# Kernel tuning notes

Hardware: AMD Instinct MI355X
Metric: run time of the kernel (lower is better)

## Reference

```python
import jax, jax.numpy as jnp
import numpy as np

K, T, F = 30000, 48, 4
EPS = 1e-5  # torch BatchNorm1d default eps


def _bn_params(key, c):
    k1, k2, k3, k4 = jax.random.split(key, 4)
    g = jax.random.uniform(k1, (c,), jnp.float32, 0.5, 1.5)
    b = jax.random.normal(k2, (c,), jnp.float32) * 0.1
    m = jax.random.normal(k3, (c,), jnp.float32) * 0.1
    v = jax.random.uniform(k4, (c,), jnp.float32, 0.5, 1.5)
    return g, b, m, v


def setup_inputs() -> dict:
    key = jax.random.key(0)
    ks = jax.random.split(key, 12)
    features = jax.random.normal(ks[0], (K, T, F), jnp.float32)
    # at least 1 valid point per non-empty voxel
    num_voxels = jnp.maximum(jax.random.randint(ks[1], (K,), 0, T), 1).astype(jnp.int32)
    coors = jax.random.randint(ks[2], (K, 3), 0, 100).astype(jnp.int32)
    # VFE1: in=8 (4 + 3 rel + 1 dist), units = 32//2 = 16
    w1 = jax.random.normal(ks[3], (8, 16), jnp.float32) / np.sqrt(8)
    b1 = jax.random.normal(ks[4], (16,), jnp.float32) * 0.01
    g1, be1, m1, v1 = _bn_params(ks[5], 16)
    # VFE2: in=32, units = 128//2 = 64
    w2 = jax.random.normal(ks[6], (32, 64), jnp.float32) / np.sqrt(32)
    b2 = jax.random.normal(ks[7], (64,), jnp.float32) * 0.01
    g2, be2, m2, v2 = _bn_params(ks[8], 64)
    # final linear 128 -> 128
    w3 = jax.random.normal(ks[9], (128, 128), jnp.float32) / np.sqrt(128)
    b3 = jax.random.normal(ks[10], (128,), jnp.float32) * 0.01
    g3, be3, m3, v3 = _bn_params(ks[11], 128)
    return dict(features=features, num_voxels=num_voxels, coors=coors,
                w1=w1, b1=b1, g1=g1, be1=be1, m1=m1, v1=v1,
                w2=w2, b2=b2, g2=g2, be2=be2, m2=m2, v2=v2,
                w3=w3, b3=b3, g3=g3, be3=be3, m3=m3, v3=v3)


def _bn(x, g, b, m, v):
    # eval-mode BatchNorm over last (channel) axis
    return (x - m) * (g / jnp.sqrt(v + EPS)) + b


def _vfe(x, W, b, g, be, m, v):
    # x: [K, T, Cin] -> [K, T, 2*units]
    h = jax.nn.relu(_bn(jnp.einsum('ktc,cu->ktu', x, W) + b, g, be, m, v))
    agg = jnp.max(h, axis=1, keepdims=True)  # [K, 1, U]
    return jnp.concatenate([h, jnp.broadcast_to(agg, h.shape)], axis=2)


def reference(features, num_voxels, coors,
              w1, b1, g1, be1, m1, v1,
              w2, b2, g2, be2, m2, v2,
              w3, b3, g3, be3, m3, v3):
    xyz = features[:, :, :3]
    nv = num_voxels.astype(features.dtype)[:, None, None]
    points_mean = jnp.sum(xyz, axis=1, keepdims=True) / nv
    rel = xyz - points_mean
    dist = jnp.linalg.norm(xyz, axis=2, keepdims=True)
    x = jnp.concatenate([features, rel, dist], axis=-1)  # [K, T, 8]
    mask = (jnp.arange(T)[None, :] < num_voxels[:, None]).astype(features.dtype)[:, :, None]
    x = x * mask
    x = _vfe(x, w1, b1, g1, be1, m1, v1) * mask   # [K, T, 32]
    x = _vfe(x, w2, b2, g2, be2, m2, v2) * mask   # [K, T, 128]
    x = jax.nn.relu(_bn(jnp.einsum('ktc,cu->ktu', x, w3) + b3, g3, be3, m3, v3)) * mask
    return jnp.max(x, axis=1)  # [K, 128]
```

## Files before the change

### kernel.cpp

```cpp
#include <hip/hip_runtime.h>

constexpr float EPS = 1e-5f;

typedef __attribute__((ext_vector_type(8))) short bf16x8;
typedef __attribute__((ext_vector_type(4))) float f32x4;

#define W2P_OFF 32768
#define W1P_OFF 40960
#define B1_OFF  41984
#define B2_OFF  42048
#define B3_OFF  42304

#define APAD 20

__device__ __forceinline__ ushort f2bf(float x) {
    union { float f; unsigned u; } a; a.f = x;
    unsigned r = a.u + 0x7fffu + ((a.u >> 16) & 1u);
    return (ushort)(r >> 16);
}

__device__ __forceinline__ unsigned cvtpk(float lo, float hi) {
    unsigned r;
    asm("v_cvt_pk_bf16_f32 %0, %1, %2" : "=v"(r) : "v"(lo), "v"(hi));
    return r;
}

__global__ void vfe_prep(
    const float* __restrict__ w1, const float* __restrict__ b1,
    const float* __restrict__ g1, const float* __restrict__ be1,
    const float* __restrict__ m1, const float* __restrict__ v1,
    const float* __restrict__ w2, const float* __restrict__ b2,
    const float* __restrict__ g2, const float* __restrict__ be2,
    const float* __restrict__ m2, const float* __restrict__ v2,
    const float* __restrict__ w3, const float* __restrict__ b3,
    const float* __restrict__ g3, const float* __restrict__ be3,
    const float* __restrict__ m3, const float* __restrict__ v3,
    void* __restrict__ ws)
{
    ushort* w3p = (ushort*)ws;
    ushort* w2p = (ushort*)((char*)ws + W2P_OFF);
    ushort* w1p = (ushort*)((char*)ws + W1P_OFF);
    float*  bb1 = (float*)((char*)ws + B1_OFF);
    float*  bb2 = (float*)((char*)ws + B2_OFF);
    float*  bb3 = (float*)((char*)ws + B3_OFF);

    const int i = blockIdx.x * 256 + threadIdx.x;
    if (i < 16384) {
        const int e = i & 7, l = (i >> 3) & 63, rest = i >> 9;
        const int ks = rest & 3, nt = rest >> 2, g = l >> 4;
        const int k = ks * 32 + g * 8 + e;
        const int n = nt * 16 + (l & 15);
        const float s = g3[n] * rsqrtf(v3[n] + EPS);
        w3p[i] = f2bf(w3[k * 128 + n] * s);
    } else if (i < 20480) {
        const int j = i - 16384;
        const int e = j & 7, l = (j >> 3) & 63, rest = j >> 9;
        const int nt = rest & 3, sel = rest >> 2;
        const int klog = (l >> 4) * 8 + e;
        const int n = nt * 16 + (l & 15);
        const float s = g2[n] * rsqrtf(v2[n] + EPS);
        w2p[j] = (klog < 16) ? f2bf(w2[(sel * 16 + klog) * 64 + n] * s) : (ushort)0;
    } else if (i < 20992) {
        const int j = i - 20480;
        const int e = j & 7, l = j >> 3;
        const int klog = (l >> 4) * 8 + e;
        const int u = l & 15;
        const float s = g1[u] * rsqrtf(v1[u] + EPS);
        w1p[j] = (klog < 8) ? f2bf(w1[klog * 16 + u] * s) : (ushort)0;
    } else if (i < 21200) {
        const int j = i - 20992;
        if (j < 16) {
            const int u = j;
            bb1[u] = (b1[u] - m1[u]) * (g1[u] * rsqrtf(v1[u] + EPS)) + be1[u];
        } else if (j < 80) {
            const int u = j - 16;
            bb2[u] = (b2[u] - m2[u]) * (g2[u] * rsqrtf(v2[u] + EPS)) + be2[u];
        } else {
            const int u = j - 80;
            bb3[u] = (b3[u] - m3[u]) * (g3[u] * rsqrtf(v3[u] + EPS)) + be3[u];
        }
    }
}

#define NV(v)   ((v)==0?nv0:(v)==1?nv1:(v)==2?nv2:nv3)
#define LIM(v)  ((v)==0?lim0:(v)==1?lim1:(v)==2?lim2:lim3)
#define FULL(v) ((v)==0?full0:(v)==1?full1:(v)==2?full2:full3)

__global__ __launch_bounds__(256, 4) void vfe_fused(
    const float* __restrict__ feat,
    const int* __restrict__ nvox,
    const void* __restrict__ ws,
    float* __restrict__ out,
    int K)
{
    __shared__ __align__(16) ushort sBfrag[12 * 2 * 64 * 8];
    __shared__ __align__(16) ushort sAfrag[12 * 16 * APAD];
    __shared__ __align__(16) ushort sAgg1bf[4][16];
    __shared__ __align__(16) ushort sAgg2bf[4][64];

    ushort (*sX0bf)[8] = (ushort(*)[8])&sBfrag[0];

    const ushort* w3p = (const ushort*)ws;
    const ushort* w2p = (const ushort*)((const char*)ws + W2P_OFF);
    const ushort* w1p = (const ushort*)((const char*)ws + W1P_OFF);
    const float*  bb1 = (const float*)((const char*)ws + B1_OFF);
    const float*  bb2 = (const float*)((const char*)ws + B2_OFF);
    const float*  bb3 = (const float*)((const char*)ws + B3_OFF);

    const int tid  = threadIdx.x;
    const int lane = tid & 63;
    const int w    = tid >> 6;
    const int g    = lane >> 4;
    const int m15  = lane & 15;
    const int kA   = blockIdx.x * 4;

    int kk0 = kA, kk1 = min(kA+1, K-1), kk2 = min(kA+2, K-1), kk3 = min(kA+3, K-1);
    int nv0 = __builtin_amdgcn_readfirstlane(nvox[kk0]);
    int nv1 = __builtin_amdgcn_readfirstlane(nvox[kk1]);
    int nv2 = __builtin_amdgcn_readfirstlane(nvox[kk2]);
    int nv3 = __builtin_amdgcn_readfirstlane(nvox[kk3]);
    const int lim0=(nv0+15)>>4, lim1=(nv1+15)>>4, lim2=(nv2+15)>>4, lim3=(nv3+15)>>4;
    const int full0=nv0>>4, full1=nv1>>4, full2=nv2>>4, full3=nv3>>4;

    union U8 { bf16x8 v; unsigned u[4]; };

    {
        const int kkw = (w==0)?kk0:(w==1)?kk1:(w==2)?kk2:kk3;
        const int nvw = (w==0)?nv0:(w==1)?nv1:(w==2)?nv2:nv3;
        float4 f = make_float4(0.f, 0.f, 0.f, 0.f);
        if (lane < 48)
            f = *reinterpret_cast<const float4*>(feat + ((size_t)kkw * 48 + lane) * 4);
        float sx = f.x, sy = f.y, sz = f.z;
        #pragma unroll
        for (int d = 1; d < 64; d <<= 1) {
            sx += __shfl_xor(sx, d);
            sy += __shfl_xor(sy, d);
            sz += __shfl_xor(sz, d);
        }
        const float inv = 1.f / (float)nvw;
        if (lane < 48) {
            const float msk = (lane < nvw) ? 1.f : 0.f;
            const float dd = sqrtf(f.x * f.x + f.y * f.y + f.z * f.z);
            U8 a;
            a.u[0] = cvtpk(f.x * msk, f.y * msk);
            a.u[1] = cvtpk(f.z * msk, f.w * msk);
            a.u[2] = cvtpk((f.x - sx * inv) * msk, (f.y - sy * inv) * msk);
            a.u[3] = cvtpk((f.z - sz * inv) * msk, dd * msk);
            *reinterpret_cast<bf16x8*>(&sX0bf[w * 48 + lane][0]) = a.v;
        }
    }

    {
        const bf16x8 b1f = *(const bf16x8*)(w1p + (size_t)lane * 8);
        const float bb1u = bb1[m15];
        const int limw = (w==0)?lim0:(w==1)?lim1:(w==2)?lim2:lim3;
        const f32x4 ci = {bb1u, bb1u, bb1u, bb1u};
        float pmax = fmaxf(bb1u, 0.f);
        #pragma unroll
        for (int s = 0; s < 3; ++s) {
            if (s < limw) {
                const bf16x8 af = *(const bf16x8*)&sX0bf[w * 48 + s * 16 + m15][0];
                f32x4 acc = __builtin_amdgcn_mfma_f32_16x16x32_bf16(af, b1f, ci, 0, 0, 0);
                float h0 = fmaxf(acc[0], 0.f), h1 = fmaxf(acc[1], 0.f);
                float h2 = fmaxf(acc[2], 0.f), h3 = fmaxf(acc[3], 0.f);
                pmax = fmaxf(pmax, fmaxf(fmaxf(h0, h1), fmaxf(h2, h3)));
                const unsigned p01 = cvtpk(h0, h1), p23 = cvtpk(h2, h3);
                ushort* base = &sAfrag[((w * 3 + s) * 16 + g * 4) * APAD + m15];
                base[0 * APAD] = (ushort)p01;
                base[1 * APAD] = (ushort)(p01 >> 16);
                base[2 * APAD] = (ushort)p23;
                base[3 * APAD] = (ushort)(p23 >> 16);
            }
        }
        pmax = fmaxf(pmax, __shfl_xor(pmax, 16));
        pmax = fmaxf(pmax, __shfl_xor(pmax, 32));
        if (g == 0) sAgg1bf[w][m15] = f2bf(pmax);
    }
    __syncthreads();

    const int col2 = w * 16 + m15;
    const float bb2c = bb2[col2];
    f32x4 z2acc;
    {
        const bf16x8 w2hif = *(const bf16x8*)(w2p + (size_t)((1 * 4 + w) * 64 + lane) * 8);
        const bf16x8 az2 = *(const bf16x8*)&sAgg1bf[m15 & 3][(g & 1) * 8];
        f32x4 ci = {bb2c, bb2c, bb2c, bb2c};
        z2acc = __builtin_amdgcn_mfma_f32_16x16x32_bf16(az2, w2hif, ci, 0, 0, 0);
    }

    {
        const bf16x8 w2lof = *(const bf16x8*)(w2p + (size_t)((0 * 4 + w) * 64 + lane) * 8);
        const int ks = col2 >> 5, gp = (col2 >> 3) & 3, e = col2 & 7;
        #pragma unroll
        for (int vg = 0; vg < 2; ++vg) {
            const f32x4 cP = {z2acc[vg*2],   z2acc[vg*2],   z2acc[vg*2],   z2acc[vg*2]};
            const f32x4 cQ = {z2acc[vg*2+1], z2acc[vg*2+1], z2acc[vg*2+1], z2acc[vg*2+1]};
            f32x4 acc2[6];
            #pragma unroll
            for (int j = 0; j < 6; ++j) {
                const int tt = vg * 6 + j;
                const int vox = vg * 2 + j / 3;
                const int mtl = j % 3;
                if (mtl < LIM(vox)) {
                    const bf16x8 af = *(const bf16x8*)&sAfrag[(tt * 16 + m15) * APAD + (g & 1) * 8];
                    acc2[j] = __builtin_amdgcn_mfma_f32_16x16x32_bf16(af, w2lof, (j < 3) ? cP : cQ, 0, 0, 0);
                }
            }
            float mxP = fmaxf(bb2c, 0.f);
            float mxQ = fmaxf(bb2c, 0.f);
            #pragma unroll
            for (int j = 0; j < 6; ++j) {
                const int tt = vg * 6 + j;
                const int vox = vg * 2 + j / 3;
                const int mtl = j % 3;
                if (mtl < LIM(vox)) {
                    float h[4];
                    #pragma unroll
                    for (int r = 0; r < 4; ++r) h[r] = fmaxf(acc2[j][r], 0.f);
                    const unsigned p01 = cvtpk(h[0], h[1]), p23 = cvtpk(h[2], h[3]);
                    ushort* base = &sBfrag[((tt * 2 + ks) * 64 + gp * 16 + g * 4) * 8 + e];
                    base[0]  = (ushort)p01;
                    base[8]  = (ushort)(p01 >> 16);
                    base[16] = (ushort)p23;
                    base[24] = (ushort)(p23 >> 16);
                    if (mtl < FULL(vox)) {
                        const float t01 = fmaxf(h[0], h[1]), t23 = fmaxf(h[2], h[3]);
                        if (j < 3) mxP = fmaxf(mxP, fmaxf(t01, t23));
                        else       mxQ = fmaxf(mxQ, fmaxf(t01, t23));
                    } else {
                        #pragma unroll
                        for (int r = 0; r < 4; ++r) {
                            if (mtl * 16 + g * 4 + r < NV(vox)) {
                                if (j < 3) mxP = fmaxf(mxP, h[r]);
                                else       mxQ = fmaxf(mxQ, h[r]);
                            }
                        }
                    }
                }
            }
            mxP = fmaxf(mxP, __shfl_xor(mxP, 16));
            mxP = fmaxf(mxP, __shfl_xor(mxP, 32));
            mxQ = fmaxf(mxQ, __shfl_xor(mxQ, 16));
            mxQ = fmaxf(mxQ, __shfl_xor(mxQ, 32));
            if (g == 0) {
                sAgg2bf[vg * 2 + 0][col2] = f2bf(mxP);
                sAgg2bf[vg * 2 + 1][col2] = f2bf(mxQ);
            }
        }
    }
    __syncthreads();

    f32x4 i3[2];
    {
        bf16x8 b3h[2][2];
        #pragma unroll
        for (int nt = 0; nt < 2; ++nt)
            #pragma unroll
            for (int ks2 = 0; ks2 < 2; ++ks2)
                b3h[nt][ks2] = *(const bf16x8*)(w3p + (size_t)(((w * 2 + nt) * 4 + 2 + ks2) * 64 + lane) * 8);
        #pragma unroll
        for (int nt = 0; nt < 2; ++nt) {
            const float bb3c = bb3[(w * 2 + nt) * 16 + m15];
            f32x4 z = {bb3c, bb3c, bb3c, bb3c};
            #pragma unroll
            for (int ks2 = 0; ks2 < 2; ++ks2) {
                const bf16x8 af = *(const bf16x8*)&sAgg2bf[m15 & 3][ks2 * 32 + g * 8];
                z = __builtin_amdgcn_mfma_f32_16x16x32_bf16(af, b3h[nt][ks2], z, 0, 0, 0);
            }
            i3[nt] = z;
        }
    }

    #pragma unroll
    for (int pass = 0; pass < 2; ++pass) {
        const int col = (w * 2 + pass) * 16 + m15;
        bf16x8 b3l[2];
        #pragma unroll
        for (int ks2 = 0; ks2 < 2; ++ks2)
            b3l[ks2] = *(const bf16x8*)(w3p + (size_t)(((w * 2 + pass) * 4 + ks2) * 64 + lane) * 8);
        #pragma unroll
        for (int vg = 0; vg < 2; ++vg) {
            const f32x4 cP = {i3[pass][vg*2],   i3[pass][vg*2],   i3[pass][vg*2],   i3[pass][vg*2]};
            const f32x4 cQ = {i3[pass][vg*2+1], i3[pass][vg*2+1], i3[pass][vg*2+1], i3[pass][vg*2+1]};
            f32x4 acc3[6];
            __builtin_amdgcn_s_setprio(1);
            #pragma unroll
            for (int j = 0; j < 6; ++j) {
                const int tt = vg * 6 + j;
                const int vox = vg * 2 + j / 3;
                const int mtl = j % 3;
                if (mtl < LIM(vox)) {
                    const bf16x8 af0 = *(const bf16x8*)&sBfrag[((tt * 2 + 0) * 64 + lane) * 8];
                    const bf16x8 af1 = *(const bf16x8*)&sBfrag[((tt * 2 + 1) * 64 + lane) * 8];
                    acc3[j] = __builtin_amdgcn_mfma_f32_16x16x32_bf16(af0, b3l[0], (j < 3) ? cP : cQ, 0, 0, 0);
                    acc3[j] = __builtin_amdgcn_mfma_f32_16x16x32_bf16(af1, b3l[1], acc3[j], 0, 0, 0);
                }
            }
            __builtin_amdgcn_s_setprio(0);
            float mxP = 0.f, mxQ = 0.f;
            #pragma unroll
            for (int j = 0; j < 6; ++j) {
                const int vox = vg * 2 + j / 3;
                const int mtl = j % 3;
                if (mtl < FULL(vox)) {
                    const float t01 = fmaxf(acc3[j][0], acc3[j][1]);
                    const float t23 = fmaxf(acc3[j][2], acc3[j][3]);
                    if (j < 3) mxP = fmaxf(mxP, fmaxf(t01, t23));
                    else       mxQ = fmaxf(mxQ, fmaxf(t01, t23));
                } else if (mtl < LIM(vox)) {
                    #pragma unroll
                    for (int r = 0; r < 4; ++r) {
                        if (mtl * 16 + g * 4 + r < NV(vox)) {
                            if (j < 3) mxP = fmaxf(mxP, acc3[j][r]);
                            else       mxQ = fmaxf(mxQ, acc3[j][r]);
                        }
                    }
                }
            }
            mxP = fmaxf(mxP, __shfl_xor(mxP, 16));
            mxP = fmaxf(mxP, __shfl_xor(mxP, 32));
            mxQ = fmaxf(mxQ, __shfl_xor(mxQ, 16));
            mxQ = fmaxf(mxQ, __shfl_xor(mxQ, 32));
            if (g == (vg * 2 + 0) && (kA + vg * 2 + 0) < K) out[(size_t)(kA + vg * 2 + 0) * 128 + col] = mxP;
            if (g == (vg * 2 + 1) && (kA + vg * 2 + 1) < K) out[(size_t)(kA + vg * 2 + 1) * 128 + col] = mxQ;
        }
    }
}

extern "C" void kernel_launch(void* const* d_in, const int* in_sizes, int n_in,
                              void* d_out, int out_size, void* d_ws, size_t ws_size,
                              hipStream_t stream) {
    const float* feat = (const float*)d_in[0];
    const int*   nvx  = (const int*)d_in[1];
    const float* w1 = (const float*)d_in[3];
    const float* b1 = (const float*)d_in[4];
    const float* g1 = (const float*)d_in[5];
    const float* be1= (const float*)d_in[6];
    const float* m1 = (const float*)d_in[7];
    const float* v1 = (const float*)d_in[8];
    const float* w2 = (const float*)d_in[9];
    const float* b2 = (const float*)d_in[10];
    const float* g2 = (const float*)d_in[11];
    const float* be2= (const float*)d_in[12];
    const float* m2 = (const float*)d_in[13];
    const float* v2 = (const float*)d_in[14];
    const float* w3 = (const float*)d_in[15];
    const float* b3 = (const float*)d_in[16];
    const float* g3 = (const float*)d_in[17];
    const float* be3= (const float*)d_in[18];
    const float* m3 = (const float*)d_in[19];
    const float* v3 = (const float*)d_in[20];
    float* out = (float*)d_out;

    const int K = in_sizes[1];

    vfe_prep<<<84, 256, 0, stream>>>(w1,b1,g1,be1,m1,v1, w2,b2,g2,be2,m2,v2,
                                     w3,b3,g3,be3,m3,v3, d_ws);
    vfe_fused<<<(K + 3) / 4, 256, 0, stream>>>(feat, nvx, d_ws, out, K);
}
```

Baseline: 73.75 us.

## Halve shared-memory footprint by phasing layer-2/3 per voxel pair, raise occupancy

Restructures the layer-2 and layer-3 stages into two phases, each handling a pair of voxels. The activation buffer in shared memory only needs 6 tiles instead of 12, which allows launch bounds of 8 blocks per SM instead of 4. The A-fragment padding also drops from 20 to 16. The aim is more resident waves to hide latency, at the cost of extra barriers per block, a tighter register budget, and possible LDS bank conflicts without the padding.

```diff
diff --git a/kernel.cpp b/kernel.cpp
--- a/kernel.cpp
+++ b/kernel.cpp
@@ -11,7 +11,7 @@
 #define B2_OFF  42048
 #define B3_OFF  42304
 
-#define APAD 20
+#define APAD 16
 
 __device__ __forceinline__ ushort f2bf(float x) {
     union { float f; unsigned u; } a; a.f = x;
@@ -86,14 +86,14 @@
 #define LIM(v)  ((v)==0?lim0:(v)==1?lim1:(v)==2?lim2:lim3)
 #define FULL(v) ((v)==0?full0:(v)==1?full1:(v)==2?full2:full3)
 
-__global__ __launch_bounds__(256, 4) void vfe_fused(
+__global__ __launch_bounds__(256, 8) void vfe_fused(
     const float* __restrict__ feat,
     const int* __restrict__ nvox,
     const void* __restrict__ ws,
     float* __restrict__ out,
     int K)
 {
-    __shared__ __align__(16) ushort sBfrag[12 * 2 * 64 * 8];
+    __shared__ __align__(16) ushort sBfrag[6 * 2 * 64 * 8];
     __shared__ __align__(16) ushort sAfrag[12 * 16 * APAD];
     __shared__ __align__(16) ushort sAgg1bf[4][16];
     __shared__ __align__(16) ushort sAgg2bf[4][64];
@@ -187,38 +187,41 @@
         f32x4 ci = {bb2c, bb2c, bb2c, bb2c};
         z2acc = __builtin_amdgcn_mfma_f32_16x16x32_bf16(az2, w2hif, ci, 0, 0, 0);
     }
-
-    {
-        const bf16x8 w2lof = *(const bf16x8*)(w2p + (size_t)((0 * 4 + w) * 64 + lane) * 8);
-        const int ks = col2 >> 5, gp = (col2 >> 3) & 3, e = col2 & 7;
-        #pragma unroll
-        for (int vg = 0; vg < 2; ++vg) {
-            const f32x4 cP = {z2acc[vg*2],   z2acc[vg*2],   z2acc[vg*2],   z2acc[vg*2]};
-            const f32x4 cQ = {z2acc[vg*2+1], z2acc[vg*2+1], z2acc[vg*2+1], z2acc[vg*2+1]};
-            f32x4 acc2[6];
+    const bf16x8 w2lof = *(const bf16x8*)(w2p + (size_t)((0 * 4 + w) * 64 + lane) * 8);
+    const int ks = col2 >> 5, gp = (col2 >> 3) & 3, e = col2 & 7;
+
+    #pragma unroll
+    for (int ph = 0; ph < 2; ++ph) {
+        f32x4 acc2[6];
+        {
+            const f32x4 cP2 = {z2acc[ph*2],   z2acc[ph*2],   z2acc[ph*2],   z2acc[ph*2]};
+            const f32x4 cQ2 = {z2acc[ph*2+1], z2acc[ph*2+1], z2acc[ph*2+1], z2acc[ph*2+1]};
             #pragma unroll
             for (int j = 0; j < 6; ++j) {
-                const int tt = vg * 6 + j;
-                const int vox = vg * 2 + j / 3;
+                const int tt = ph * 6 + j;
+                const int vox = ph * 2 + j / 3;
                 const int mtl = j % 3;
                 if (mtl < LIM(vox)) {
                     const bf16x8 af = *(const bf16x8*)&sAfrag[(tt * 16 + m15) * APAD + (g & 1) * 8];
-                    acc2[j] = __builtin_amdgcn_mfma_f32_16x16x32_bf16(af, w2lof, (j < 3) ? cP : cQ, 0, 0, 0);
-                }
-            }
+                    acc2[j] = __builtin_amdgcn_mfma_f32_16x16x32_bf16(af, w2lof, (j < 3) ? cP2 : cQ2, 0, 0, 0);
+                }
+            }
+        }
+        if (ph == 1) __syncthreads();
+
+        {
             float mxP = fmaxf(bb2c, 0.f);
             float mxQ = fmaxf(bb2c, 0.f);
             #pragma unroll
             for (int j = 0; j < 6; ++j) {
-                const int tt = vg * 6 + j;
-                const int vox = vg * 2 + j / 3;
+                const int vox = ph * 2 + j / 3;
                 const int mtl = j % 3;
                 if (mtl < LIM(vox)) {
                     float h[4];
                     #pragma unroll
                     for (int r = 0; r < 4; ++r) h[r] = fmaxf(acc2[j][r], 0.f);
                     const unsigned p01 = cvtpk(h[0], h[1]), p23 = cvtpk(h[2], h[3]);
-                    ushort* base = &sBfrag[((tt * 2 + ks) * 64 + gp * 16 + g * 4) * 8 + e];
+                    ushort* base = &sBfrag[((j * 2 + ks) * 64 + gp * 16 + g * 4) * 8 + e];
                     base[0]  = (ushort)p01;
                     base[8]  = (ushort)(p01 >> 16);
                     base[16] = (ushort)p23;
@@ -243,55 +246,51 @@
             mxQ = fmaxf(mxQ, __shfl_xor(mxQ, 16));
             mxQ = fmaxf(mxQ, __shfl_xor(mxQ, 32));
             if (g == 0) {
-                sAgg2bf[vg * 2 + 0][col2] = f2bf(mxP);
-                sAgg2bf[vg * 2 + 1][col2] = f2bf(mxQ);
-            }
-        }
-    }
-    __syncthreads();
-
-    f32x4 i3[2];
-    {
-        bf16x8 b3h[2][2];
+                sAgg2bf[ph * 2 + 0][col2] = f2bf(mxP);
+                sAgg2bf[ph * 2 + 1][col2] = f2bf(mxQ);
+            }
+        }
+        __syncthreads();
+
+        f32x4 i3[2];
+        {
+            bf16x8 b3h[2][2];
+            #pragma unroll
+            for (int nt = 0; nt < 2; ++nt)
+                #pragma unroll
+                for (int ks2 = 0; ks2 < 2; ++ks2)
+                    b3h[nt][ks2] = *(const bf16x8*)(w3p + (size_t)(((w * 2 + nt) * 4 + 2 + ks2) * 64 + lane) * 8);
+            #pragma unroll
+            for (int nt = 0; nt < 2; ++nt) {
+                const float bb3c = bb3[(w * 2 + nt) * 16 + m15];
+                f32x4 z = {bb3c, bb3c, bb3c, bb3c};
+                #pragma unroll
+                for (int ks2 = 0; ks2 < 2; ++ks2) {
+                    const bf16x8 af = *(const bf16x8*)&sAgg2bf[ph * 2 + (m15 & 1)][ks2 * 32 + g * 8];
+                    z = __builtin_amdgcn_mfma_f32_16x16x32_bf16(af, b3h[nt][ks2], z, 0, 0, 0);
+                }
+                i3[nt] = z;
+            }
+        }
+
         #pragma unroll
-        for (int nt = 0; nt < 2; ++nt)
+        for (int pass = 0; pass < 2; ++pass) {
+            const int col = (w * 2 + pass) * 16 + m15;
+            bf16x8 b3l[2];
             #pragma unroll
             for (int ks2 = 0; ks2 < 2; ++ks2)
-                b3h[nt][ks2] = *(const bf16x8*)(w3p + (size_t)(((w * 2 + nt) * 4 + 2 + ks2) * 64 + lane) * 8);
-        #pragma unroll
-        for (int nt = 0; nt < 2; ++nt) {
-            const float bb3c = bb3[(w * 2 + nt) * 16 + m15];
-            f32x4 z = {bb3c, bb3c, bb3c, bb3c};
-            #pragma unroll
-            for (int ks2 = 0; ks2 < 2; ++ks2) {
-                const bf16x8 af = *(const bf16x8*)&sAgg2bf[m15 & 3][ks2 * 32 + g * 8];
-                z = __builtin_amdgcn_mfma_f32_16x16x32_bf16(af, b3h[nt][ks2], z, 0, 0, 0);
-            }
-            i3[nt] = z;
-        }
-    }
-
-    #pragma unroll
-    for (int pass = 0; pass < 2; ++pass) {
-        const int col = (w * 2 + pass) * 16 + m15;
-        bf16x8 b3l[2];
-        #pragma unroll
-        for (int ks2 = 0; ks2 < 2; ++ks2)
-            b3l[ks2] = *(const bf16x8*)(w3p + (size_t)(((w * 2 + pass) * 4 + ks2) * 64 + lane) * 8);
-        #pragma unroll
-        for (int vg = 0; vg < 2; ++vg) {
-            const f32x4 cP = {i3[pass][vg*2],   i3[pass][vg*2],   i3[pass][vg*2],   i3[pass][vg*2]};
-            const f32x4 cQ = {i3[pass][vg*2+1], i3[pass][vg*2+1], i3[pass][vg*2+1], i3[pass][vg*2+1]};
+                b3l[ks2] = *(const bf16x8*)(w3p + (size_t)(((w * 2 + pass) * 4 + ks2) * 64 + lane) * 8);
+            const f32x4 cP = {i3[pass][0], i3[pass][0], i3[pass][0], i3[pass][0]};
+            const f32x4 cQ = {i3[pass][1], i3[pass][1], i3[pass][1], i3[pass][1]};
             f32x4 acc3[6];
             __builtin_amdgcn_s_setprio(1);
             #pragma unroll
             for (int j = 0; j < 6; ++j) {
-                const int tt = vg * 6 + j;
-                const int vox = vg * 2 + j / 3;
+                const int vox = ph * 2 + j / 3;
                 const int mtl = j % 3;
                 if (mtl < LIM(vox)) {
-                    const bf16x8 af0 = *(const bf16x8*)&sBfrag[((tt * 2 + 0) * 64 + lane) * 8];
-                    const bf16x8 af1 = *(const bf16x8*)&sBfrag[((tt * 2 + 1) * 64 + lane) * 8];
+                    const bf16x8 af0 = *(const bf16x8*)&sBfrag[((j * 2 + 0) * 64 + lane) * 8];
+                    const bf16x8 af1 = *(const bf16x8*)&sBfrag[((j * 2 + 1) * 64 + lane) * 8];
                     acc3[j] = __builtin_amdgcn_mfma_f32_16x16x32_bf16(af0, b3l[0], (j < 3) ? cP : cQ, 0, 0, 0);
                     acc3[j] = __builtin_amdgcn_mfma_f32_16x16x32_bf16(af1, b3l[1], acc3[j], 0, 0, 0);
                 }
@@ -300,7 +299,7 @@
             float mxP = 0.f, mxQ = 0.f;
             #pragma unroll
             for (int j = 0; j < 6; ++j) {
-                const int vox = vg * 2 + j / 3;
+                const int vox = ph * 2 + j / 3;
                 const int mtl = j % 3;
                 if (mtl < FULL(vox)) {
                     const float t01 = fmaxf(acc3[j][0], acc3[j][1]);
@@ -321,8 +320,8 @@
             mxP = fmaxf(mxP, __shfl_xor(mxP, 32));
             mxQ = fmaxf(mxQ, __shfl_xor(mxQ, 16));
             mxQ = fmaxf(mxQ, __shfl_xor(mxQ, 32));
-            if (g == (vg * 2 + 0) && (kA + vg * 2 + 0) < K) out[(size_t)(kA + vg * 2 + 0) * 128 + col] = mxP;
-            if (g == (vg * 2 + 1) && (kA + vg * 2 + 1) < K) out[(size_t)(kA + vg * 2 + 1) * 128 + col] = mxQ;
+            if (g == 0 && (kA + ph * 2 + 0) < K) out[(size_t)(kA + ph * 2 + 0) * 128 + col] = mxP;
+            if (g == 1 && (kA + ph * 2 + 1) < K) out[(size_t)(kA + ph * 2 + 1) * 128 + col] = mxQ;
         }
     }
 }
```

New measurement: 196.2 us. +166.0%, slower.
